# Performance work log

Hardware: AMD Instinct MI355X
Metric: run time of the kernel (lower is better)

## Reference

```python
import jax, jax.numpy as jnp
import numpy as np

IN_F, OUT_F, RANK = 4096, 4096, 64
ALPHA = 128.0
SCALING = ALPHA / RANK  # 2.0
BATCH_TOKENS = 8192


def setup_inputs() -> dict:
    key = jax.random.key(0)
    k1, k2, k3, k4 = jax.random.split(key, 4)
    x = jax.random.normal(k1, (BATCH_TOKENS, IN_F), dtype=jnp.float32)
    weight = jax.random.normal(k2, (OUT_F, IN_F), dtype=jnp.float32) * 0.02
    P = jax.random.normal(k3, (OUT_F, RANK), dtype=jnp.float32) * 0.01
    Lambda = jnp.ones((RANK,), dtype=jnp.float32) * 0.01
    Q = jax.random.normal(k4, (RANK, IN_F), dtype=jnp.float32) * 0.01
    rank_mask = jnp.ones((RANK,), dtype=jnp.bool_)
    return {"x": x, "weight": weight, "P": P, "Lambda": Lambda, "Q": Q, "rank_mask": rank_mask}


def reference(x, weight, P, Lambda, Q, rank_mask):
    # active_Lambda = Lambda * mask; delta_W = (P * active_Lambda) @ Q  -> [OUT_F, IN_F]
    active_Lambda = Lambda * rank_mask.astype(Lambda.dtype)
    delta_W = (P * active_Lambda[None, :]) @ Q
    # F.linear(x, W_eff) = x @ W_eff^T
    W_eff = weight + SCALING * delta_W
    return x @ W_eff.T
```

## Files before the change

kernel.cpp:

```cpp
#include <hip/hip_runtime.h>
#include <hip/hip_bf16.h>
#include <stdint.h>

#define M_TOK 8192
#define NF    4096
#define KF    4096
#define RANK  64

typedef __attribute__((ext_vector_type(8))) short short8;
typedef __attribute__((ext_vector_type(4))) float floatx4;

typedef const uint32_t __attribute__((address_space(1)))* gp1_t;
typedef uint32_t __attribute__((address_space(3)))* lp3_t;

__device__ __forceinline__ void load_lds16(const void* g, void* l) {
  __builtin_amdgcn_global_load_lds((gp1_t)g, (lp3_t)l, 16, 0, 0);
}

#define CASTX_BLOCKS ((M_TOK * KF) / (256 * 8))
__global__ __launch_bounds__(256) void prep_all(
    const float* __restrict__ x, const float* __restrict__ W,
    const float* __restrict__ P, const float* __restrict__ Lam,
    const float* __restrict__ Q, const unsigned char* __restrict__ mask,
    __hip_bfloat16* __restrict__ Xb, __hip_bfloat16* __restrict__ Wb) {
  __shared__ float lam[RANK];
  __shared__ float plT[RANK][68];
  __shared__ float Qs[RANK][68];

  const int bid = blockIdx.x;
  const int t = threadIdx.x;

  if (bid < CASTX_BLOCKS) {
    size_t i = ((size_t)bid * 256 + t) * 8;
    float4 a = *(const float4*)(x + i);
    float4 b = *(const float4*)(x + i + 4);
    union { __hip_bfloat16 h[8]; uint4 u; } pk;
    pk.h[0] = __float2bfloat16(a.x); pk.h[1] = __float2bfloat16(a.y);
    pk.h[2] = __float2bfloat16(a.z); pk.h[3] = __float2bfloat16(a.w);
    pk.h[4] = __float2bfloat16(b.x); pk.h[5] = __float2bfloat16(b.y);
    pk.h[6] = __float2bfloat16(b.z); pk.h[7] = __float2bfloat16(b.w);
    *(uint4*)(Xb + i) = pk.u;
    return;
  }

  const int idx = bid - CASTX_BLOCKS;
  const int n0 = (idx >> 6) * 64;
  const int k0 = (idx & 63) * 64;

  if (t < RANK) lam[t] = 2.0f * Lam[t] * (mask[t] ? 1.0f : 0.0f);
  __syncthreads();

  {
    const int nl = t & 63;
    const int rg = (t >> 6) * 16;
    const float* p = P + (size_t)(n0 + nl) * RANK + rg;
#pragma unroll
    for (int j = 0; j < 16; j += 4) {
      float4 v = *(const float4*)(p + j);
      plT[rg + j + 0][nl] = v.x * lam[rg + j + 0];
      plT[rg + j + 1][nl] = v.y * lam[rg + j + 1];
      plT[rg + j + 2][nl] = v.z * lam[rg + j + 2];
      plT[rg + j + 3][nl] = v.w * lam[rg + j + 3];
    }
    const int r = t >> 2;
    const int kc = (t & 3) * 16;
    const float* q = Q + (size_t)r * KF + k0 + kc;
#pragma unroll
    for (int j = 0; j < 16; j += 4) {
      float4 v = *(const float4*)(q + j);
      Qs[r][kc + j + 0] = v.x;
      Qs[r][kc + j + 1] = v.y;
      Qs[r][kc + j + 2] = v.z;
      Qs[r][kc + j + 3] = v.w;
    }
  }
  __syncthreads();

  const int tn4 = t >> 4;
  const int tk4 = t & 15;
  float accv[4][4];
#pragma unroll
  for (int i = 0; i < 4; i++) {
    float4 w = *(const float4*)(W + (size_t)(n0 + tn4 * 4 + i) * KF + k0 + tk4 * 4);
    accv[i][0] = w.x; accv[i][1] = w.y; accv[i][2] = w.z; accv[i][3] = w.w;
  }
#pragma unroll 8
  for (int r = 0; r < RANK; r++) {
    float4 p4 = *(const float4*)&plT[r][tn4 * 4];
    float4 q4 = *(const float4*)&Qs[r][tk4 * 4];
#define ROWFMA(i, pi)                                                  \
    accv[i][0] += (pi) * q4.x; accv[i][1] += (pi) * q4.y;              \
    accv[i][2] += (pi) * q4.z; accv[i][3] += (pi) * q4.w;
    ROWFMA(0, p4.x) ROWFMA(1, p4.y) ROWFMA(2, p4.z) ROWFMA(3, p4.w)
#undef ROWFMA
  }
#pragma unroll
  for (int i = 0; i < 4; i++) {
    union { __hip_bfloat16 h[4]; uint2 u; } pk;
    pk.h[0] = __float2bfloat16(accv[i][0]);
    pk.h[1] = __float2bfloat16(accv[i][1]);
    pk.h[2] = __float2bfloat16(accv[i][2]);
    pk.h[3] = __float2bfloat16(accv[i][3]);
    *(uint2*)(Wb + (size_t)(n0 + tn4 * 4 + i) * KF + k0 + tk4 * 4) = pk.u;
  }
}

#define BM 256
#define BN 256
#define BK 64
#define NT (KF / BK)
#define ASL 16384

#define SB0 __builtin_amdgcn_sched_barrier(0)
#define BARSYNC do { SB0; __builtin_amdgcn_s_barrier(); } while (0)
#define LGK(n) do { asm volatile("s_waitcnt lgkmcnt(" #n ")" ::: "memory"); SB0; } while (0)

__device__ __forceinline__ void read_a4(short8 (&afr)[2][2],
                                        const __hip_bfloat16* Asl,
                                        int row_base, int swz) {
#pragma unroll
  for (int mm = 0; mm < 2; ++mm)
#pragma unroll
    for (int ks = 0; ks < 2; ++ks)
      afr[mm][ks] = *(const short8*)(Asl + ks * 8192 + (row_base + mm * 16) * 32 + swz);
}

__device__ __forceinline__ void read_b8(short8 (&bfr)[4][2],
                                        const __hip_bfloat16* Bsl,
                                        int brow, int swz) {
#pragma unroll
  for (int nf = 0; nf < 4; ++nf)
#pragma unroll
    for (int ks = 0; ks < 2; ++ks)
      bfr[nf][ks] = *(const short8*)(Bsl + ks * 8192 + (brow + nf * 16) * 32 + swz);
}

template <int P>
__device__ __forceinline__ void mfma16(floatx4 (&acc)[8][4],
                                       const short8 (&afr)[2][2],
                                       const short8 (&bfr)[4][2]) {
#pragma unroll
  for (int ks = 0; ks < 2; ++ks)
#pragma unroll
    for (int mm = 0; mm < 2; ++mm)
#pragma unroll
      for (int nf = 0; nf < 4; ++nf)
        acc[P * 2 + mm][nf] = __builtin_amdgcn_mfma_f32_16x16x32_bf16(
            afr[mm][ks], bfr[nf][ks], acc[P * 2 + mm][nf], 0, 0, 0);
}

__global__ __launch_bounds__(512, 2) void gemm_xwt(
    const __hip_bfloat16* __restrict__ A,
    const __hip_bfloat16* __restrict__ B,
    float* __restrict__ C) {
  extern __shared__ __hip_bfloat16 lds[];
  __hip_bfloat16* As = lds;
  __hip_bfloat16* Bs = lds + 2 * ASL;
  const __hip_bfloat16* As0 = As;
  const __hip_bfloat16* As1 = As + ASL;
  const __hip_bfloat16* Bs0 = Bs;
  const __hip_bfloat16* Bs1 = Bs + ASL;

  const int t = threadIdx.x;
  const int lane = t & 63;
  const int wave = t >> 6;
  const int wm = wave >> 2;
  const int wn = wave & 3;
  const int frow = lane & 15;
  const int kq = lane >> 4;
  const int swz = ((kq + (frow >> 1)) & 3) * 8;

  const int bid = blockIdx.x;
  const int wk = (bid & 7) * 64 + (bid >> 3);
  const int bm = wk >> 4;
  const int bn = wk & 15;

  const int c = ((t & 3) - ((t >> 3) & 3)) & 3;
  const __hip_bfloat16* a_src = A + (size_t)(bm * BM + (t >> 2)) * KF + c * 8;
  const __hip_bfloat16* b_src = B + (size_t)(bn * BN + (t >> 2)) * KF + c * 8;
  __hip_bfloat16* a_dst = As + t * 8;
  __hip_bfloat16* b_dst = Bs + t * 8;

#define STAGE_A(kt_, slot_, h_)                                                        \
  do {                                                                                 \
    const __hip_bfloat16* s_ = a_src + ((kt_) & (NT - 1)) * BK + (size_t)(h_) * 128 * KF; \
    __hip_bfloat16* d_ = a_dst + (slot_) * ASL + (h_) * 4096;                          \
    load_lds16(s_, d_);                                                \
    load_lds16(s_ + 32, d_ + 8192);                                    \
  } while (0)
#define STAGE_B(kt_, slot_, h_)                                                        \
  do {                                                                                 \
    const __hip_bfloat16* s_ = b_src + ((kt_) & (NT - 1)) * BK + (size_t)(h_) * 128 * KF; \
    __hip_bfloat16* d_ = b_dst + (slot_) * ASL + (h_) * 4096;                          \
    load_lds16(s_, d_);                                                                \
    load_lds16(s_ + 32, d_ + 8192);                                                    \
  } while (0)

  floatx4 acc[8][4] = {};
  short8 bE[4][2], bO[4][2];
  short8 aX[2][2], aY[2][2];

  const int arow = wm * 128 + frow;
  const int brow = wn * 64 + frow;

  STAGE_A(0, 0, 0); STAGE_A(0, 0, 1);
  STAGE_B(0, 0, 0); STAGE_B(0, 0, 1);
  STAGE_A(1, 1, 0); STAGE_A(1, 1, 1);
  STAGE_B(1, 1, 0); STAGE_B(1, 1, 1);
  asm volatile("s_waitcnt vmcnt(8)" ::: "memory");
  __builtin_amdgcn_s_barrier();
  read_b8(bE, Bs0, brow, swz);
  read_a4(aX, As0, arow + 0 * 32, swz);

  for (int kt = 0; kt < NT; kt += 2) {
    read_a4(aY, As0, arow + 1 * 32, swz);
    STAGE_B(kt + 2, 0, 0);
    BARSYNC; LGK(4);
    __builtin_amdgcn_s_setprio(1); mfma16<0>(acc, aX, bE); __builtin_amdgcn_s_setprio(0);
    BARSYNC;
    read_a4(aX, As0, arow + 2 * 32, swz);
    STAGE_B(kt + 2, 0, 1);
    BARSYNC; LGK(4);
    __builtin_amdgcn_s_setprio(1); mfma16<1>(acc, aY, bE); __builtin_amdgcn_s_setprio(0);
    BARSYNC;
    read_a4(aY, As0, arow + 3 * 32, swz);
    BARSYNC; LGK(4);
    __builtin_amdgcn_s_setprio(1); mfma16<2>(acc, aX, bE); __builtin_amdgcn_s_setprio(0);
    SB0;
    asm volatile("s_waitcnt vmcnt(4)" ::: "memory");
    __builtin_amdgcn_s_barrier();
    read_b8(bO, Bs1, brow, swz);
    read_a4(aX, As1, arow + 0 * 32, swz);
    BARSYNC; LGK(12);
    STAGE_A(kt + 2, 0, 0);
    STAGE_A(kt + 2, 0, 1);
    SB0;
    __builtin_amdgcn_s_setprio(1); mfma16<3>(acc, aY, bE); __builtin_amdgcn_s_setprio(0);
    BARSYNC;

    read_a4(aY, As1, arow + 1 * 32, swz);
    STAGE_B(kt + 3, 1, 0);
    BARSYNC; LGK(4);
    __builtin_amdgcn_s_setprio(1); mfma16<0>(acc, aX, bO); __builtin_amdgcn_s_setprio(0);
    BARSYNC;
    read_a4(aX, As1, arow + 2 * 32, swz);
    STAGE_B(kt + 3, 1, 1);
    BARSYNC; LGK(4);
    __builtin_amdgcn_s_setprio(1); mfma16<1>(acc, aY, bO); __builtin_amdgcn_s_setprio(0);
    BARSYNC;
    read_a4(aY, As1, arow + 3 * 32, swz);
    BARSYNC; LGK(4);
    __builtin_amdgcn_s_setprio(1); mfma16<2>(acc, aX, bO); __builtin_amdgcn_s_setprio(0);
    SB0;
    asm volatile("s_waitcnt vmcnt(4)" ::: "memory");
    __builtin_amdgcn_s_barrier();
    read_b8(bE, Bs0, brow, swz);
    read_a4(aX, As0, arow + 0 * 32, swz);
    BARSYNC; LGK(12);
    STAGE_A(kt + 3, 1, 0);
    STAGE_A(kt + 3, 1, 1);
    SB0;
    __builtin_amdgcn_s_setprio(1); mfma16<3>(acc, aY, bO); __builtin_amdgcn_s_setprio(0);
    BARSYNC;
  }

#undef STAGE_A
#undef STAGE_B

  const int col0 = bn * BN + wn * 64 + (lane & 15);
  const int row0 = bm * BM + wm * 128 + (lane >> 4) * 4;
#pragma unroll
  for (int mf = 0; mf < 8; ++mf)
#pragma unroll
    for (int nf = 0; nf < 4; ++nf)
#pragma unroll
      for (int r = 0; r < 4; ++r)
        C[(size_t)(row0 + mf * 16 + r) * NF + (col0 + nf * 16)] = acc[mf][nf][r];
}

extern "C" void kernel_launch(void* const* d_in, const int* in_sizes, int n_in,
                              void* d_out, int out_size, void* d_ws, size_t ws_size,
                              hipStream_t stream) {
  const float* x      = (const float*)d_in[0];
  const float* weight = (const float*)d_in[1];
  const float* P      = (const float*)d_in[2];
  const float* Lam    = (const float*)d_in[3];
  const float* Q      = (const float*)d_in[4];
  const unsigned char* mask = (const unsigned char*)d_in[5];
  float* out = (float*)d_out;

  __hip_bfloat16* Xb = (__hip_bfloat16*)d_ws;
  __hip_bfloat16* Wb = (__hip_bfloat16*)((char*)d_ws + (size_t)M_TOK * KF * 2);

  static int smem_set = 0;
  if (!smem_set) {
    hipFuncSetAttribute((const void*)gemm_xwt,
                        hipFuncAttributeMaxDynamicSharedMemorySize, 131072);
    smem_set = 1;
  }

  prep_all<<<CASTX_BLOCKS + (NF / 64) * (KF / 64), 256, 0, stream>>>(
      x, weight, P, Lam, Q, mask, Xb, Wb);
  gemm_xwt<<<dim3((M_TOK / BM) * (NF / BN)), 512, 131072, stream>>>(Xb, Wb, out);
}
```

Baseline: 517.0 us.

## Switch GEMM to 32x32x16 MFMA and rebalance A/B staging schedule

Replaces the 16x16x32 bf16 MFMA tiles with 32x32x16 MFMA, changing the fragment layout, the LDS read pattern and swizzle, and the output store mapping. Staging of the A tile for the next K step is interleaved with the B loads across the MFMA phases instead of being issued in bursts, and the vmcnt waits are adjusted to match. Larger MFMA tiles need fewer LDS fragment reads per flop and fewer instruction issues. The rescheduled waits risk ordering hazards, and the accumulator register layout changes.

```diff
diff --git a/kernel.cpp b/kernel.cpp
--- a/kernel.cpp
+++ b/kernel.cpp
@@ -8,7 +8,7 @@
 #define RANK  64
 
 typedef __attribute__((ext_vector_type(8))) short short8;
-typedef __attribute__((ext_vector_type(4))) float floatx4;
+typedef __attribute__((ext_vector_type(16))) float floatx16;
 
 typedef const uint32_t __attribute__((address_space(1)))* gp1_t;
 typedef uint32_t __attribute__((address_space(3)))* lp3_t;
@@ -115,38 +115,34 @@
 #define BARSYNC do { SB0; __builtin_amdgcn_s_barrier(); } while (0)
 #define LGK(n) do { asm volatile("s_waitcnt lgkmcnt(" #n ")" ::: "memory"); SB0; } while (0)
 
-__device__ __forceinline__ void read_a4(short8 (&afr)[2][2],
-                                        const __hip_bfloat16* Asl,
-                                        int row_base, int swz) {
-#pragma unroll
-  for (int mm = 0; mm < 2; ++mm)
-#pragma unroll
-    for (int ks = 0; ks < 2; ++ks)
-      afr[mm][ks] = *(const short8*)(Asl + ks * 8192 + (row_base + mm * 16) * 32 + swz);
-}
-
-__device__ __forceinline__ void read_b8(short8 (&bfr)[4][2],
-                                        const __hip_bfloat16* Bsl,
-                                        int brow, int swz) {
-#pragma unroll
-  for (int nf = 0; nf < 4; ++nf)
-#pragma unroll
-    for (int ks = 0; ks < 2; ++ks)
-      bfr[nf][ks] = *(const short8*)(Bsl + ks * 8192 + (brow + nf * 16) * 32 + swz);
-}
-
-template <int P>
-__device__ __forceinline__ void mfma16(floatx4 (&acc)[8][4],
-                                       const short8 (&afr)[2][2],
-                                       const short8 (&bfr)[4][2]) {
-#pragma unroll
-  for (int ks = 0; ks < 2; ++ks)
-#pragma unroll
-    for (int mm = 0; mm < 2; ++mm)
-#pragma unroll
-      for (int nf = 0; nf < 4; ++nf)
-        acc[P * 2 + mm][nf] = __builtin_amdgcn_mfma_f32_16x16x32_bf16(
-            afr[mm][ks], bfr[nf][ks], acc[P * 2 + mm][nf], 0, 0, 0);
+__device__ __forceinline__ void read_a32(short8 (&afr)[4],
+                                         const __hip_bfloat16* Asl,
+                                         int row, const int (&pc)[4]) {
+#pragma unroll
+  for (int ks = 0; ks < 4; ++ks)
+    afr[ks] = *(const short8*)(Asl + (ks >> 1) * 8192 + row * 32 + pc[ks] * 8);
+}
+
+__device__ __forceinline__ void read_b32(short8 (&bfr)[2][4],
+                                         const __hip_bfloat16* Bsl,
+                                         int row, const int (&pc)[4]) {
+#pragma unroll
+  for (int nj = 0; nj < 2; ++nj)
+#pragma unroll
+    for (int ks = 0; ks < 4; ++ks)
+      bfr[nj][ks] = *(const short8*)(Bsl + (ks >> 1) * 8192 + (row + nj * 32) * 32 + pc[ks] * 8);
+}
+
+template <int MI>
+__device__ __forceinline__ void mfma8(floatx16 (&acc)[4][2],
+                                      const short8 (&afr)[4],
+                                      const short8 (&bfr)[2][4]) {
+#pragma unroll
+  for (int ks = 0; ks < 4; ++ks)
+#pragma unroll
+    for (int nj = 0; nj < 2; ++nj)
+      acc[MI][nj] = __builtin_amdgcn_mfma_f32_32x32x16_bf16(
+          afr[ks], bfr[nj][ks], acc[MI][nj], 0, 0, 0);
 }
 
 __global__ __launch_bounds__(512, 2) void gemm_xwt(
@@ -166,9 +162,13 @@
   const int wave = t >> 6;
   const int wm = wave >> 2;
   const int wn = wave & 3;
-  const int frow = lane & 15;
-  const int kq = lane >> 4;
-  const int swz = ((kq + (frow >> 1)) & 3) * 8;
+  const int l31 = lane & 31;
+  const int lhi = lane >> 5;
+
+  int pc[4];
+#pragma unroll
+  for (int ks = 0; ks < 4; ++ks)
+    pc[ks] = ((ks & 1) * 2 + lhi + ((l31 >> 1) & 3)) & 3;
 
   const int bid = blockIdx.x;
   const int wk = (bid & 7) * 64 + (bid >> 3);
@@ -196,86 +196,84 @@
     load_lds16(s_ + 32, d_ + 8192);                                                    \
   } while (0)
 
-  floatx4 acc[8][4] = {};
-  short8 bE[4][2], bO[4][2];
-  short8 aX[2][2], aY[2][2];
-
-  const int arow = wm * 128 + frow;
-  const int brow = wn * 64 + frow;
+  floatx16 acc[4][2] = {};
+  short8 bE[2][4], bO[2][4];
+  short8 aX[4], aY[4];
+
+  const int rowA = wm * 128 + l31;
+  const int rowB = wn * 64 + l31;
 
   STAGE_A(0, 0, 0); STAGE_A(0, 0, 1);
   STAGE_B(0, 0, 0); STAGE_B(0, 0, 1);
-  STAGE_A(1, 1, 0); STAGE_A(1, 1, 1);
   STAGE_B(1, 1, 0); STAGE_B(1, 1, 1);
-  asm volatile("s_waitcnt vmcnt(8)" ::: "memory");
+  asm volatile("s_waitcnt vmcnt(4)" ::: "memory");
   __builtin_amdgcn_s_barrier();
-  read_b8(bE, Bs0, brow, swz);
-  read_a4(aX, As0, arow + 0 * 32, swz);
+  read_b32(bE, Bs0, rowB, pc);
+  read_a32(aX, As0, rowA + 0 * 32, pc);
 
   for (int kt = 0; kt < NT; kt += 2) {
-    read_a4(aY, As0, arow + 1 * 32, swz);
+    read_a32(aY, As0, rowA + 1 * 32, pc);
+    STAGE_A(kt + 1, 1, 0);
+    BARSYNC; LGK(4);
+    __builtin_amdgcn_s_setprio(1); mfma8<0>(acc, aX, bE); __builtin_amdgcn_s_setprio(0);
+    BARSYNC;
+    read_a32(aX, As0, rowA + 2 * 32, pc);
+    STAGE_A(kt + 1, 1, 1);
+    BARSYNC; LGK(4);
+    __builtin_amdgcn_s_setprio(1); mfma8<1>(acc, aY, bE); __builtin_amdgcn_s_setprio(0);
+    BARSYNC;
+    read_a32(aY, As0, rowA + 3 * 32, pc);
     STAGE_B(kt + 2, 0, 0);
     BARSYNC; LGK(4);
-    __builtin_amdgcn_s_setprio(1); mfma16<0>(acc, aX, bE); __builtin_amdgcn_s_setprio(0);
-    BARSYNC;
-    read_a4(aX, As0, arow + 2 * 32, swz);
+    __builtin_amdgcn_s_setprio(1); mfma8<2>(acc, aX, bE); __builtin_amdgcn_s_setprio(0);
+    SB0;
+    asm volatile("s_waitcnt vmcnt(2)" ::: "memory");
+    __builtin_amdgcn_s_barrier();
+    read_b32(bO, Bs1, rowB, pc);
+    read_a32(aX, As1, rowA + 0 * 32, pc);
     STAGE_B(kt + 2, 0, 1);
-    BARSYNC; LGK(4);
-    __builtin_amdgcn_s_setprio(1); mfma16<1>(acc, aY, bE); __builtin_amdgcn_s_setprio(0);
-    BARSYNC;
-    read_a4(aY, As0, arow + 3 * 32, swz);
-    BARSYNC; LGK(4);
-    __builtin_amdgcn_s_setprio(1); mfma16<2>(acc, aX, bE); __builtin_amdgcn_s_setprio(0);
+    BARSYNC; LGK(12);
+    __builtin_amdgcn_s_setprio(1); mfma8<3>(acc, aY, bE); __builtin_amdgcn_s_setprio(0);
+    BARSYNC;
+
+    read_a32(aY, As1, rowA + 1 * 32, pc);
+    STAGE_A(kt + 2, 0, 0);
+    BARSYNC; LGK(4);
+    __builtin_amdgcn_s_setprio(1); mfma8<0>(acc, aX, bO); __builtin_amdgcn_s_setprio(0);
+    BARSYNC;
+    read_a32(aX, As1, rowA + 2 * 32, pc);
+    STAGE_A(kt + 2, 0, 1);
+    BARSYNC; LGK(4);
+    __builtin_amdgcn_s_setprio(1); mfma8<1>(acc, aY, bO); __builtin_amdgcn_s_setprio(0);
+    BARSYNC;
+    read_a32(aY, As1, rowA + 3 * 32, pc);
+    STAGE_B(kt + 3, 1, 0);
+    BARSYNC; LGK(4);
+    __builtin_amdgcn_s_setprio(1); mfma8<2>(acc, aX, bO); __builtin_amdgcn_s_setprio(0);
     SB0;
-    asm volatile("s_waitcnt vmcnt(4)" ::: "memory");
+    asm volatile("s_waitcnt vmcnt(2)" ::: "memory");
     __builtin_amdgcn_s_barrier();
-    read_b8(bO, Bs1, brow, swz);
-    read_a4(aX, As1, arow + 0 * 32, swz);
+    read_b32(bE, Bs0, rowB, pc);
+    read_a32(aX, As0, rowA + 0 * 32, pc);
+    STAGE_B(kt + 3, 1, 1);
     BARSYNC; LGK(12);
-    STAGE_A(kt + 2, 0, 0);
-    STAGE_A(kt + 2, 0, 1);
-    SB0;
-    __builtin_amdgcn_s_setprio(1); mfma16<3>(acc, aY, bE); __builtin_amdgcn_s_setprio(0);
-    BARSYNC;
-
-    read_a4(aY, As1, arow + 1 * 32, swz);
-    STAGE_B(kt + 3, 1, 0);
-    BARSYNC; LGK(4);
-    __builtin_amdgcn_s_setprio(1); mfma16<0>(acc, aX, bO); __builtin_amdgcn_s_setprio(0);
-    BARSYNC;
-    read_a4(aX, As1, arow + 2 * 32, swz);
-    STAGE_B(kt + 3, 1, 1);
-    BARSYNC; LGK(4);
-    __builtin_amdgcn_s_setprio(1); mfma16<1>(acc, aY, bO); __builtin_amdgcn_s_setprio(0);
-    BARSYNC;
-    read_a4(aY, As1, arow + 3 * 32, swz);
-    BARSYNC; LGK(4);
-    __builtin_amdgcn_s_setprio(1); mfma16<2>(acc, aX, bO); __builtin_amdgcn_s_setprio(0);
-    SB0;
-    asm volatile("s_waitcnt vmcnt(4)" ::: "memory");
-    __builtin_amdgcn_s_barrier();
-    read_b8(bE, Bs0, brow, swz);
-    read_a4(aX, As0, arow + 0 * 32, swz);
-    BARSYNC; LGK(12);
-    STAGE_A(kt + 3, 1, 0);
-    STAGE_A(kt + 3, 1, 1);
-    SB0;
-    __builtin_amdgcn_s_setprio(1); mfma16<3>(acc, aY, bO); __builtin_amdgcn_s_setprio(0);
+    __builtin_amdgcn_s_setprio(1); mfma8<3>(acc, aY, bO); __builtin_amdgcn_s_setprio(0);
     BARSYNC;
   }
 
 #undef STAGE_A
 #undef STAGE_B
 
-  const int col0 = bn * BN + wn * 64 + (lane & 15);
-  const int row0 = bm * BM + wm * 128 + (lane >> 4) * 4;
-#pragma unroll
-  for (int mf = 0; mf < 8; ++mf)
-#pragma unroll
-    for (int nf = 0; nf < 4; ++nf)
-#pragma unroll
-      for (int r = 0; r < 4; ++r)
-        C[(size_t)(row0 + mf * 16 + r) * NF + (col0 + nf * 16)] = acc[mf][nf][r];
+  const int col0 = bn * BN + wn * 64 + l31;
+  const int row0 = bm * BM + wm * 128 + 4 * lhi;
+#pragma unroll
+  for (int mi = 0; mi < 4; ++mi)
+#pragma unroll
+    for (int nj = 0; nj < 2; ++nj)
+#pragma unroll
+      for (int r = 0; r < 16; ++r)
+        C[(size_t)(row0 + mi * 32 + (r & 3) + 8 * (r >> 2)) * NF +
+          (col0 + nj * 32)] = acc[mi][nj][r];
 }
 
 extern "C" void kernel_launch(void* const* d_in, const int* in_sizes, int n_in,
```

Result: slower. 528.1 us (+2.2%).
